# Performance work log

Hardware: AMD Instinct MI355X
Metric: run time of the kernel (lower is better)

Reference implementation:

```python
import jax, jax.numpy as jnp
import numpy as np

DROPOUT_P = 0.3


def setup_inputs() -> dict:
    key = jax.random.key(0)
    kq, kk, kv, ks = jax.random.split(key, 4)
    B, Sq, Skv, D = 32, 2048, 2048, 128
    q = jax.random.normal(kq, (B, Sq, D), dtype=jnp.float32)
    k = jax.random.normal(kk, (B, Skv, D), dtype=jnp.float32)
    v = jax.random.normal(kv, (B, Skv, D), dtype=jnp.float32)
    # torch.randint(low=1, high=256, size=[B,1]) -> per-batch positive scale
    scale_factor = jax.random.randint(ks, (B, 1, 1), 1, 256).astype(jnp.float32)
    return {"q": q, "k": k, "v": v, "scale_factor": scale_factor}


def reference(q, k, v, scale_factor):
    # qk = q @ k^T ; div by scale_factor**-1 == multiply by scale_factor
    scores = jnp.einsum("bqd,bkd->bqk", q, k) * scale_factor  # [B,Sq,Skv]
    attn = jax.nn.softmax(scores, axis=-1)
    # dropout with fixed key (deterministic reference for torch F.dropout)
    keep_p = 1.0 - DROPOUT_P
    dk = jax.random.key(42)
    keep = jax.random.bernoulli(dk, keep_p, attn.shape)
    attn_d = jnp.where(keep, attn / keep_p, 0.0)
    return jnp.einsum("bqk,bkd->bqd", attn_d, v)
```

## Files before the change

kernel.cpp:

```cpp
#include <hip/hip_runtime.h>
#include <stdint.h>


namespace {

constexpr int Bb  = 32;
constexpr int SQ  = 2048;
constexpr int SKV = 2048;
constexpr int DH  = 128;
constexpr int KT  = 32;
constexpr int NKT = SKV / KT;
constexpr int TILE_F16 = 12288;
constexpr size_t WS_NEED = (size_t)Bb * NKT * TILE_F16 * 2;
constexpr int PSTR = KT + 8;

typedef _Float16 f16x8 __attribute__((ext_vector_type(8)));
typedef _Float16 f16x4 __attribute__((ext_vector_type(4)));
typedef float    f32x4 __attribute__((ext_vector_type(4)));

__device__ __forceinline__ uint32_t rotl32(uint32_t x, int d) {
  return (x << d) | (x >> (32 - d));
}

__device__ __forceinline__ uint32_t jax_random_bits(uint32_t i) {
  constexpr uint32_t K0 = 0u;
  constexpr uint32_t K1 = 42u;
  constexpr uint32_t K2 = 0x1BD11BDAu ^ K0 ^ K1;
  uint32_t x0 = K0;
  uint32_t x1 = i + K1;
#define TF4(a,b,c,d) \
  x0 += x1; x1 = rotl32(x1,a); x1 ^= x0; \
  x0 += x1; x1 = rotl32(x1,b); x1 ^= x0; \
  x0 += x1; x1 = rotl32(x1,c); x1 ^= x0; \
  x0 += x1; x1 = rotl32(x1,d); x1 ^= x0;
  TF4(13,15,26,6)   x0 += K1; x1 += K2 + 1u;
  TF4(17,29,16,24)  x0 += K2; x1 += K0 + 2u;
  TF4(13,15,26,6)   x0 += K0; x1 += K1 + 3u;
  TF4(17,29,16,24)  x0 += K1; x1 += K2 + 4u;
  TF4(13,15,26,6)   x0 += K2; x1 += K0 + 5u;
#undef TF4
  return x0 ^ x1;
}

__device__ __forceinline__ bool jax_keep_bits(uint32_t bits) {
  return (bits >> 9) < 0x0059999Au;
}

__device__ __forceinline__ _Float16 hi16(float x) { return (_Float16)x; }
__device__ __forceinline__ _Float16 lo16(float x) {
  return (_Float16)(x - (float)((_Float16)x));
}

template <int CTRL>
__device__ __forceinline__ float dppf(float v) {
  return __int_as_float(__builtin_amdgcn_update_dpp(
      0, __float_as_int(v), CTRL, 0xF, 0xF, true));
}
__device__ __forceinline__ float row16_max(float x) {
  x = fmaxf(x, dppf<0xB1>(x));
  x = fmaxf(x, dppf<0x4E>(x));
  x = fmaxf(x, dppf<0x141>(x));
  x = fmaxf(x, dppf<0x140>(x));
  return x;
}
__device__ __forceinline__ float row16_sum(float x) {
  x += dppf<0xB1>(x);
  x += dppf<0x4E>(x);
  x += dppf<0x141>(x);
  x += dppf<0x140>(x);
  return x;
}

}

__global__ __launch_bounds__(256) void prep_tile(const float* __restrict__ Kg,
                                                 const float* __restrict__ Vg,
                                                 _Float16* __restrict__ ws) {
  __shared__ alignas(16) float sT[KT][DH + 4];

  const int tid  = threadIdx.x;
  const int b    = blockIdx.x >> 6;
  const int kt   = blockIdx.x & 63;
  _Float16* tile = ws + (size_t)(b * NKT + kt) * TILE_F16;

  float4 vreg[4];
  {
    const float* kb = Kg + ((size_t)b * SKV + kt * KT) * DH;
    const float* vb = Vg + ((size_t)b * SKV + kt * KT) * DH;
#pragma unroll
    for (int rep = 0; rep < 4; ++rep) {
      const int idx = tid + 256 * rep;
      const int row = idx >> 5;
      const int c4  = idx & 31;
      *reinterpret_cast<float4*>(&sT[row][4 * c4]) =
          *reinterpret_cast<const float4*>(kb + (size_t)row * DH + 4 * c4);
      vreg[rep] = *reinterpret_cast<const float4*>(vb + (size_t)row * DH + 4 * c4);
    }
  }
  __syncthreads();
#pragma unroll
  for (int rep = 0; rep < 2; ++rep) {
    const int task = tid + 256 * rep;
    const int lane = task & 63;
    const int f    = task >> 6;
    const int ks   = f >> 1;
    const int ct   = f & 1;
    const int cl   = lane & 15;
    const int g8   = (lane >> 4) * 8;
    const float* src = &sT[ct * 16 + cl][ks * 32 + g8];
    f16x8 h, l;
#pragma unroll
    for (int j = 0; j < 8; ++j) { h[j] = hi16(src[j]); l[j] = lo16(src[j]); }
    *reinterpret_cast<f16x8*>(tile + f * 512 + lane * 8)        = h;
    *reinterpret_cast<f16x8*>(tile + 4096 + f * 512 + lane * 8) = l;
  }
  __syncthreads();

#pragma unroll
  for (int rep = 0; rep < 4; ++rep) {
    const int idx = tid + 256 * rep;
    const int row = idx >> 5;
    const int c4  = idx & 31;
    *reinterpret_cast<float4*>(&sT[row][4 * c4]) = vreg[rep];
  }
  __syncthreads();
#pragma unroll
  for (int rep = 0; rep < 2; ++rep) {
    const int task = tid + 256 * rep;
    const int lane = task & 63;
    const int dt   = task >> 6;
    const int cl   = lane & 15;
    const int g8   = (lane >> 4) * 8;
    f16x8 w;
#pragma unroll
    for (int j = 0; j < 8; ++j)
      w[j] = (_Float16)sT[g8 + j][dt * 16 + cl];
    *reinterpret_cast<f16x8*>(tile + 8192 + dt * 512 + lane * 8) = w;
  }
}

__global__ __launch_bounds__(256, 3) void fused_attn5(
    const float* __restrict__ Qg, const _Float16* __restrict__ Wk,
    const float* __restrict__ Sg, float* __restrict__ Og)
{
  __shared__ alignas(16) _Float16 sStage[TILE_F16];
  __shared__ alignas(16) _Float16 sP[4][16][PSTR];

  const int tid  = threadIdx.x;
  const int wid  = tid >> 6;
  const int lane = tid & 63;
  const int cl   = lane & 15;
  const int g8   = (lane >> 4) * 8;
  const int r0   = (lane >> 4) * 4;

  const int b  = blockIdx.x >> 5;
  const int q0 = (blockIdx.x & 31) * 64;
  const float scale = Sg[b];

  f16x8 qhi[4], qlo[4];
  {
    const float* qp = Qg + ((size_t)b * SQ + q0 + wid * 16 + cl) * DH + g8;
#pragma unroll
    for (int ks = 0; ks < 4; ++ks) {
      const float4 a0 = *reinterpret_cast<const float4*>(qp + 32 * ks);
      const float4 a1 = *reinterpret_cast<const float4*>(qp + 32 * ks + 4);
      const float xs[8] = {a0.x, a0.y, a0.z, a0.w, a1.x, a1.y, a1.z, a1.w};
#pragma unroll
      for (int j = 0; j < 8; ++j) { qhi[ks][j] = hi16(xs[j]); qlo[ks][j] = lo16(xs[j]); }
    }
  }

  float m_run[4], l_run[4], alpha[4];
  f32x4 oacc[8];
#pragma unroll
  for (int i = 0; i < 4; ++i) { m_run[i] = -INFINITY; l_run[i] = 0.0f; }
#pragma unroll
  for (int dt = 0; dt < 8; ++dt) oacc[dt] = (f32x4){0.f, 0.f, 0.f, 0.f};

  for (int kt = 0; kt < NKT; ++kt) {
    __syncthreads();

    const uint32_t* tsrc =
        reinterpret_cast<const uint32_t*>(Wk + (size_t)(b * NKT + kt) * TILE_F16);
#pragma unroll
    for (int c = 0; c < 6; ++c) {
      const int j = wid + 4 * c;
      __builtin_amdgcn_global_load_lds(tsrc + j * 256 + lane * 4,
          reinterpret_cast<uint32_t*>(&sStage[j * 512]), 16, 0, 0);
    }
    __syncthreads();

    f32x4 sacc[2];
    __builtin_amdgcn_s_setprio(1);
#pragma unroll
    for (int ct = 0; ct < 2; ++ct) {
      sacc[ct] = (f32x4){0.f, 0.f, 0.f, 0.f};
#pragma unroll
      for (int ks = 0; ks < 4; ++ks) {
        const int f = ks * 2 + ct;
        const f16x8 bhi = *reinterpret_cast<const f16x8*>(&sStage[f * 512 + lane * 8]);
        const f16x8 blo = *reinterpret_cast<const f16x8*>(&sStage[4096 + f * 512 + lane * 8]);
        sacc[ct] = __builtin_amdgcn_mfma_f32_16x16x32_f16(qhi[ks], bhi, sacc[ct], 0, 0, 0);
        sacc[ct] = __builtin_amdgcn_mfma_f32_16x16x32_f16(qlo[ks], bhi, sacc[ct], 0, 0, 0);
        sacc[ct] = __builtin_amdgcn_mfma_f32_16x16x32_f16(qhi[ks], blo, sacc[ct], 0, 0, 0);
      }
    }
    __builtin_amdgcn_s_setprio(0);

    bool anyalpha = false;
    bool tk[4];
#pragma unroll
    for (int i = 0; i < 4; ++i) {
      const float mraw = row16_max(fmaxf(sacc[0][i], sacc[1][i]));
      const float mt = mraw * scale;

      tk[i] = (mt >= m_run[i] - 9.21f);
      if (tk[i]) {
        const float mnew = fmaxf(m_run[i], mt);
        alpha[i] = __expf(m_run[i] - mnew);
        m_run[i] = mnew;
        const int qrow = q0 + wid * 16 + r0 + i;
        const uint32_t rowbase =
            ((uint32_t)b * (uint32_t)SQ + (uint32_t)qrow) * (uint32_t)SKV
            + (uint32_t)(kt * KT);

        const float t0 = sacc[0][i] * scale - mnew;
        const float t1 = sacc[1][i] * scale - mnew;
        const float p0 = __expf(t0);
        const float p1 = __expf(t1);
        const float ps = row16_sum(p0 + p1);
        l_run[i] = l_run[i] * alpha[i] + ps;
        anyalpha |= (alpha[i] != 1.0f);

        if (__any(t0 >= -17.75f)) {
          const uint32_t bits = jax_random_bits(rowbase + (uint32_t)cl);
          sP[wid][r0 + i][cl] = jax_keep_bits(bits)
                                    ? (_Float16)(p0 * (1.0f / 0.7f))
                                    : (_Float16)0.0f;
        } else {
          sP[wid][r0 + i][cl] = (_Float16)0.0f;
        }
        if (__any(t1 >= -17.75f)) {
          const uint32_t bits = jax_random_bits(rowbase + (uint32_t)(16 + cl));
          sP[wid][r0 + i][16 + cl] = jax_keep_bits(bits)
                                         ? (_Float16)(p1 * (1.0f / 0.7f))
                                         : (_Float16)0.0f;
        } else {
          sP[wid][r0 + i][16 + cl] = (_Float16)0.0f;
        }
      } else {
        alpha[i] = 1.0f;
      }
    }

    const int myAllSkip = !(tk[0] || tk[1] || tk[2] || tk[3]);
    if (!__all(myAllSkip)) {
#pragma unroll
      for (int i = 0; i < 4; ++i) {
        if (!tk[i]) {
#pragma unroll
          for (int ct = 0; ct < 2; ++ct)
            sP[wid][r0 + i][16 * ct + cl] = (_Float16)0.0f;
        }
      }

      if (anyalpha) {
#pragma unroll
        for (int dt = 0; dt < 8; ++dt)
#pragma unroll
          for (int i = 0; i < 4; ++i) oacc[dt][i] *= alpha[i];
      }

      const f16x8 pa = *reinterpret_cast<const f16x8*>(&sP[wid][cl][g8]);
      __builtin_amdgcn_s_setprio(1);
#pragma unroll
      for (int dt = 0; dt < 8; ++dt) {
        const f16x8 bv = *reinterpret_cast<const f16x8*>(
            &sStage[8192 + dt * 512 + lane * 8]);
        oacc[dt] = __builtin_amdgcn_mfma_f32_16x16x32_f16(pa, bv, oacc[dt], 0, 0, 0);
      }
      __builtin_amdgcn_s_setprio(0);
    }
  }

#pragma unroll
  for (int i = 0; i < 4; ++i) {
    const float inv_l = 1.0f / l_run[i];
    float* op = Og + ((size_t)b * SQ + (size_t)(q0 + wid * 16 + r0 + i)) * DH + cl;
#pragma unroll
    for (int dt = 0; dt < 8; ++dt)
      op[16 * dt] = oacc[dt][i] * inv_l;
  }
}

namespace {
constexpr int FKT  = 64;
constexpr int KSTR = DH + 8;
constexpr int VSTR = FKT + 8;
constexpr int FPSTR = FKT + 8;
}

__global__ __launch_bounds__(256, 2) void fused_attn_fb(
    const float* __restrict__ Qg, const float* __restrict__ Kg,
    const float* __restrict__ Vg, const float* __restrict__ Sg,
    float* __restrict__ Og)
{
  __shared__ alignas(16) _Float16 sKhi[FKT][KSTR];
  __shared__ alignas(16) _Float16 sKlo[FKT][KSTR];
  __shared__ alignas(16) _Float16 sVt[DH][VSTR];
  __shared__ alignas(16) _Float16 sP[4][16][FPSTR];

  const int tid  = threadIdx.x;
  const int wid  = tid >> 6;
  const int lane = tid & 63;
  const int cl   = lane & 15;
  const int g8   = (lane >> 4) * 8;
  const int r0   = (lane >> 4) * 4;

  const int b  = blockIdx.x >> 5;
  const int q0 = (blockIdx.x & 31) * 64;
  const float scale = Sg[b];

  f16x8 qhi[4], qlo[4];
  {
    const float* qp = Qg + ((size_t)b * SQ + q0 + wid * 16 + cl) * DH + g8;
#pragma unroll
    for (int ks = 0; ks < 4; ++ks) {
      const float4 a0 = *reinterpret_cast<const float4*>(qp + 32 * ks);
      const float4 a1 = *reinterpret_cast<const float4*>(qp + 32 * ks + 4);
      const float xs[8] = {a0.x, a0.y, a0.z, a0.w, a1.x, a1.y, a1.z, a1.w};
#pragma unroll
      for (int j = 0; j < 8; ++j) { qhi[ks][j] = hi16(xs[j]); qlo[ks][j] = lo16(xs[j]); }
    }
  }

  float m_run[4], l_run[4], alpha[4];
  f32x4 oacc[8];
#pragma unroll
  for (int i = 0; i < 4; ++i) { m_run[i] = -INFINITY; l_run[i] = 0.0f; }
#pragma unroll
  for (int dt = 0; dt < 8; ++dt) oacc[dt] = (f32x4){0.f, 0.f, 0.f, 0.f};

  for (int k0 = 0; k0 < SKV; k0 += FKT) {
    __syncthreads();
#pragma unroll
    for (int rep = 0; rep < 8; ++rep) {
      const int idx = tid + 256 * rep;
      const int row = idx >> 5;
      const int c4  = idx & 31;
      const float4 t = *reinterpret_cast<const float4*>(
          Kg + ((size_t)b * SKV + k0 + row) * DH + 4 * c4);
      f16x4 h4, l4;
      h4[0] = hi16(t.x); l4[0] = lo16(t.x);
      h4[1] = hi16(t.y); l4[1] = lo16(t.y);
      h4[2] = hi16(t.z); l4[2] = lo16(t.z);
      h4[3] = hi16(t.w); l4[3] = lo16(t.w);
      *reinterpret_cast<f16x4*>(&sKhi[row][4 * c4]) = h4;
      *reinterpret_cast<f16x4*>(&sKlo[row][4 * c4]) = l4;
    }
#pragma unroll
    for (int rep = 0; rep < 2; ++rep) {
      const int u  = tid + 256 * rep;
      const int du = u & 31;
      const int ku = u >> 5;
      const float* vb = Vg + ((size_t)b * SKV + k0 + 4 * ku) * DH + 4 * du;
      float4 t[4];
#pragma unroll
      for (int j = 0; j < 4; ++j)
        t[j] = *reinterpret_cast<const float4*>(vb + (size_t)j * DH);
#pragma unroll
      for (int dd = 0; dd < 4; ++dd) {
        const float v0 = (&t[0].x)[dd], v1 = (&t[1].x)[dd],
                    v2 = (&t[2].x)[dd], v3 = (&t[3].x)[dd];
        f16x4 w4 = {(_Float16)v0, (_Float16)v1, (_Float16)v2, (_Float16)v3};
        *reinterpret_cast<f16x4*>(&sVt[4 * du + dd][4 * ku]) = w4;
      }
    }
    __syncthreads();

    f32x4 sacc[4];
#pragma unroll
    for (int ct = 0; ct < 4; ++ct) {
      sacc[ct] = (f32x4){0.f, 0.f, 0.f, 0.f};
#pragma unroll
      for (int ks = 0; ks < 4; ++ks) {
        const f16x8 bhi = *reinterpret_cast<const f16x8*>(&sKhi[16 * ct + cl][32 * ks + g8]);
        const f16x8 blo = *reinterpret_cast<const f16x8*>(&sKlo[16 * ct + cl][32 * ks + g8]);
        sacc[ct] = __builtin_amdgcn_mfma_f32_16x16x32_f16(qhi[ks], bhi, sacc[ct], 0, 0, 0);
        sacc[ct] = __builtin_amdgcn_mfma_f32_16x16x32_f16(qlo[ks], bhi, sacc[ct], 0, 0, 0);
        sacc[ct] = __builtin_amdgcn_mfma_f32_16x16x32_f16(qhi[ks], blo, sacc[ct], 0, 0, 0);
      }
    }

    bool anyalpha = false;
#pragma unroll
    for (int i = 0; i < 4; ++i) {
      float mraw = fmaxf(fmaxf(sacc[0][i], sacc[1][i]), fmaxf(sacc[2][i], sacc[3][i]));
#pragma unroll
      for (int off = 8; off >= 1; off >>= 1)
        mraw = fmaxf(mraw, __shfl_xor(mraw, off, 64));
      const float mt = mraw * scale;
      if (mt >= m_run[i] - 9.21f) {
        const float mnew = fmaxf(m_run[i], mt);
        alpha[i] = __expf(m_run[i] - mnew);
        m_run[i] = mnew;
        const int qrow = q0 + wid * 16 + r0 + i;
        const uint32_t rowbase =
            ((uint32_t)b * (uint32_t)SQ + (uint32_t)qrow) * (uint32_t)SKV + (uint32_t)k0;
        float ps = 0.0f;
#pragma unroll
        for (int ct = 0; ct < 4; ++ct) {
          const float p = __expf(sacc[ct][i] * scale - mnew);
          ps += p;
          const bool keep = jax_keep_bits(jax_random_bits(rowbase + (uint32_t)(16 * ct + cl)));
          sP[wid][r0 + i][16 * ct + cl] = keep ? (_Float16)(p * (1.0f / 0.7f))
                                               : (_Float16)0.0f;
        }
#pragma unroll
        for (int off = 8; off >= 1; off >>= 1)
          ps += __shfl_xor(ps, off, 64);
        l_run[i] = l_run[i] * alpha[i] + ps;
        anyalpha |= (alpha[i] != 1.0f);
      } else {
        alpha[i] = 1.0f;
#pragma unroll
        for (int ct = 0; ct < 4; ++ct)
          sP[wid][r0 + i][16 * ct + cl] = (_Float16)0.0f;
      }
    }

    if (anyalpha) {
#pragma unroll
      for (int dt = 0; dt < 8; ++dt)
#pragma unroll
        for (int i = 0; i < 4; ++i) oacc[dt][i] *= alpha[i];
    }
#pragma unroll
    for (int ks2 = 0; ks2 < 2; ++ks2) {
      const f16x8 pa = *reinterpret_cast<const f16x8*>(&sP[wid][cl][32 * ks2 + g8]);
#pragma unroll
      for (int dt = 0; dt < 8; ++dt) {
        const f16x8 bv = *reinterpret_cast<const f16x8*>(&sVt[16 * dt + cl][32 * ks2 + g8]);
        oacc[dt] = __builtin_amdgcn_mfma_f32_16x16x32_f16(pa, bv, oacc[dt], 0, 0, 0);
      }
    }
  }

#pragma unroll
  for (int i = 0; i < 4; ++i) {
    const float inv_l = 1.0f / l_run[i];
    float* op = Og + ((size_t)b * SQ + (size_t)(q0 + wid * 16 + r0 + i)) * DH + cl;
#pragma unroll
    for (int dt = 0; dt < 8; ++dt)
      op[16 * dt] = oacc[dt][i] * inv_l;
  }
}

extern "C" void kernel_launch(void* const* d_in, const int* in_sizes, int n_in,
                              void* d_out, int out_size, void* d_ws, size_t ws_size,
                              hipStream_t stream) {
  (void)in_sizes; (void)n_in; (void)out_size;
  const float* q  = (const float*)d_in[0];
  const float* k  = (const float*)d_in[1];
  const float* v  = (const float*)d_in[2];
  const float* sc = (const float*)d_in[3];
  float* out = (float*)d_out;

  if (ws_size >= WS_NEED) {
    _Float16* ws = (_Float16*)d_ws;
    prep_tile<<<dim3(Bb * NKT), dim3(256), 0, stream>>>(k, v, ws);
    fused_attn5<<<dim3(Bb * (SQ / 64)), dim3(256), 0, stream>>>(q, ws, sc, out);
  } else {
    fused_attn_fb<<<dim3(Bb * (SQ / 64)), dim3(256), 0, stream>>>(q, k, v, sc, out);
  }
}
```

Measured before the change: 336.4 us.

## Swizzle prep_tile LDS layout, skip redundant zero stores and alpha exp

The K/V staging buffer in prep_tile now uses an XOR swizzle on float4 columns, so the transposed and strided reads avoid LDS bank conflicts. The K reads become float4 vector loads. V loads are moved after the K conversion instead of being held in registers. In the attention kernel, the alpha exp is computed only when the running max actually increases. Rows whose sP entries are already zero are no longer re-zeroed, which removes redundant LDS stores at the cost of an extra per-row flag.

```diff
diff --git a/kernel.cpp b/kernel.cpp
--- a/kernel.cpp
+++ b/kernel.cpp
@@ -71,6 +71,8 @@
   return x;
 }
 
+__device__ __forceinline__ int swz8(int row) { return (row + (row >> 3)) & 7; }
+
 }
 
 __global__ __launch_bounds__(256) void prep_tile(const float* __restrict__ Kg,
@@ -83,18 +85,15 @@
   const int kt   = blockIdx.x & 63;
   _Float16* tile = ws + (size_t)(b * NKT + kt) * TILE_F16;
 
-  float4 vreg[4];
   {
     const float* kb = Kg + ((size_t)b * SKV + kt * KT) * DH;
-    const float* vb = Vg + ((size_t)b * SKV + kt * KT) * DH;
 #pragma unroll
     for (int rep = 0; rep < 4; ++rep) {
       const int idx = tid + 256 * rep;
       const int row = idx >> 5;
       const int c4  = idx & 31;
-      *reinterpret_cast<float4*>(&sT[row][4 * c4]) =
+      *reinterpret_cast<float4*>(&sT[row][4 * (c4 ^ swz8(row))]) =
           *reinterpret_cast<const float4*>(kb + (size_t)row * DH + 4 * c4);
-      vreg[rep] = *reinterpret_cast<const float4*>(vb + (size_t)row * DH + 4 * c4);
     }
   }
   __syncthreads();
@@ -107,21 +106,31 @@
     const int ct   = f & 1;
     const int cl   = lane & 15;
     const int g8   = (lane >> 4) * 8;
-    const float* src = &sT[ct * 16 + cl][ks * 32 + g8];
+    const int rowk = ct * 16 + cl;
+    const int c4a  = ks * 8 + (g8 >> 2);
+    const float4 xa = *reinterpret_cast<const float4*>(
+        &sT[rowk][4 * (c4a ^ swz8(rowk))]);
+    const float4 xb = *reinterpret_cast<const float4*>(
+        &sT[rowk][4 * ((c4a + 1) ^ swz8(rowk))]);
+    const float xs[8] = {xa.x, xa.y, xa.z, xa.w, xb.x, xb.y, xb.z, xb.w};
     f16x8 h, l;
 #pragma unroll
-    for (int j = 0; j < 8; ++j) { h[j] = hi16(src[j]); l[j] = lo16(src[j]); }
+    for (int j = 0; j < 8; ++j) { h[j] = hi16(xs[j]); l[j] = lo16(xs[j]); }
     *reinterpret_cast<f16x8*>(tile + f * 512 + lane * 8)        = h;
     *reinterpret_cast<f16x8*>(tile + 4096 + f * 512 + lane * 8) = l;
   }
   __syncthreads();
 
-#pragma unroll
-  for (int rep = 0; rep < 4; ++rep) {
-    const int idx = tid + 256 * rep;
-    const int row = idx >> 5;
-    const int c4  = idx & 31;
-    *reinterpret_cast<float4*>(&sT[row][4 * c4]) = vreg[rep];
+  {
+    const float* vb = Vg + ((size_t)b * SKV + kt * KT) * DH;
+#pragma unroll
+    for (int rep = 0; rep < 4; ++rep) {
+      const int idx = tid + 256 * rep;
+      const int row = idx >> 5;
+      const int c4  = idx & 31;
+      *reinterpret_cast<float4*>(&sT[row][4 * (c4 ^ swz8(row))]) =
+          *reinterpret_cast<const float4*>(vb + (size_t)row * DH + 4 * c4);
+    }
   }
   __syncthreads();
 #pragma unroll
@@ -131,10 +140,13 @@
     const int dt   = task >> 6;
     const int cl   = lane & 15;
     const int g8   = (lane >> 4) * 8;
+    const int c4v  = dt * 4 + (cl >> 2);
     f16x8 w;
 #pragma unroll
-    for (int j = 0; j < 8; ++j)
-      w[j] = (_Float16)sT[g8 + j][dt * 16 + cl];
+    for (int j = 0; j < 8; ++j) {
+      const int rowv = g8 + j;
+      w[j] = (_Float16)sT[rowv][4 * (c4v ^ swz8(rowv)) + (cl & 3)];
+    }
     *reinterpret_cast<f16x8*>(tile + 8192 + dt * 512 + lane * 8) = w;
   }
 }
@@ -171,9 +183,12 @@
   }
 
   float m_run[4], l_run[4], alpha[4];
+  bool  zknown[4];
   f32x4 oacc[8];
 #pragma unroll
-  for (int i = 0; i < 4; ++i) { m_run[i] = -INFINITY; l_run[i] = 0.0f; }
+  for (int i = 0; i < 4; ++i) {
+    m_run[i] = -INFINITY; l_run[i] = 0.0f; zknown[i] = false;
+  }
 #pragma unroll
   for (int dt = 0; dt < 8; ++dt) oacc[dt] = (f32x4){0.f, 0.f, 0.f, 0.f};
 
@@ -216,9 +231,16 @@
 
       tk[i] = (mt >= m_run[i] - 9.21f);
       if (tk[i]) {
-        const float mnew = fmaxf(m_run[i], mt);
-        alpha[i] = __expf(m_run[i] - mnew);
-        m_run[i] = mnew;
+        float mnew;
+        if (mt > m_run[i]) {
+          alpha[i] = __expf(m_run[i] - mt);
+          mnew = mt;
+          m_run[i] = mt;
+          anyalpha |= (alpha[i] != 1.0f);
+        } else {
+          alpha[i] = 1.0f;
+          mnew = m_run[i];
+        }
         const int qrow = q0 + wid * 16 + r0 + i;
         const uint32_t rowbase =
             ((uint32_t)b * (uint32_t)SQ + (uint32_t)qrow) * (uint32_t)SKV
@@ -230,7 +252,6 @@
         const float p1 = __expf(t1);
         const float ps = row16_sum(p0 + p1);
         l_run[i] = l_run[i] * alpha[i] + ps;
-        anyalpha |= (alpha[i] != 1.0f);
 
         if (__any(t0 >= -17.75f)) {
           const uint32_t bits = jax_random_bits(rowbase + (uint32_t)cl);
@@ -248,6 +269,7 @@
         } else {
           sP[wid][r0 + i][16 + cl] = (_Float16)0.0f;
         }
+        zknown[i] = false;
       } else {
         alpha[i] = 1.0f;
       }
@@ -257,10 +279,11 @@
     if (!__all(myAllSkip)) {
 #pragma unroll
       for (int i = 0; i < 4; ++i) {
-        if (!tk[i]) {
+        if (!tk[i] && !zknown[i]) {
 #pragma unroll
           for (int ct = 0; ct < 2; ++ct)
             sP[wid][r0 + i][16 * ct + cl] = (_Float16)0.0f;
+          zknown[i] = true;
         }
       }
 
```

After: 319.8 us, median of 2. 1.05x faster.
